# Optimization experiments

Hardware: AMD Instinct MI355X
Metric: run time of the kernel (lower is better)

Reference implementation:

```python
import jax, jax.numpy as jnp
import numpy as np

BLOCKSIZE = 128
KEEPER = 128


def setup_inputs() -> dict:
    key = jax.random.key(0)
    ks = jax.random.split(key, 8)
    S, H = 2048, 4096
    n_nonout = H - KEEPER          # 3968
    nb = n_nonout // BLOCKSIZE     # 31 low-precision blocks
    return {
        "x": jax.random.normal(ks[0], (1, S, H), dtype=jnp.float32),
        "weight": jax.random.normal(ks[1], (H, H), dtype=jnp.float32),   # [out, in]
        "scales": jax.random.uniform(ks[2], (H, n_nonout), dtype=jnp.float32),
        "keep_scales": jax.random.uniform(ks[3], (H, 1), dtype=jnp.float32),
        "inp_scales_lo": jax.random.uniform(ks[4], (S, nb), dtype=jnp.float32),
        "inp_scales_hi": jax.random.uniform(ks[5], (S, 1), dtype=jnp.float32),
        "inp_base_lo": jax.random.uniform(ks[6], (S, nb), dtype=jnp.float32),
        "inp_base_hi": jax.random.uniform(ks[7], (S, 1), dtype=jnp.float32),
    }


def reference(x, weight, scales, keep_scales, inp_scales_lo, inp_scales_hi,
              inp_base_lo, inp_base_hi):
    # Faithful vectorization of QLinearLayer._forward (channel_group == 0, bias None).
    bs, S, H = x.shape
    xs = x[0]                      # [S, H]  (bs == 1 assert in original)
    W = weight.T                   # [H, O]
    n_nonout = H - KEEPER
    nb = n_nonout // BLOCKSIZE
    O = W.shape[1]

    # Per-block weight scales: scales[:, i1] for each block start i1 -> [nb, O]
    w_blk_scales = scales[:, 0:n_nonout:BLOCKSIZE].T              # [nb, O]

    # Blockwise outer-product scaling fused into the operands:
    # y[s,o] = sum_n sc_lo[s,n] * ws[n,o] * (x_block_n @ W_block_n)[s,o]
    x_lo = xs[:, :n_nonout].reshape(S, nb, BLOCKSIZE) * inp_scales_lo[:, :, None]
    W_lo = W[:n_nonout, :].reshape(nb, BLOCKSIZE, O) * w_blk_scales[:, None, :]
    y = x_lo.reshape(S, n_nonout) @ W_lo.reshape(n_nonout, O)     # [S, O]

    # int8 keeper channels (high-precision path)
    hi_scales = inp_scales_hi @ keep_scales.T                      # [S, O]
    y_hi = xs[:, n_nonout:] @ W[n_nonout:, :]                      # [S, O]
    y = y + y_hi * hi_scales

    return y.reshape(bs, S, O)
```

## Files before the change

### kernel.cpp

```cpp
#include <hip/hip_runtime.h>

#define S_DIM 2048
#define K_DIM 4096
#define O_DIM 4096
#define NNON  3968
#define NB    31

#define XBLK 8192
#define WBLK 16384

typedef __bf16 bf16x8 __attribute__((ext_vector_type(8)));
typedef float  f32x4  __attribute__((ext_vector_type(4)));

__device__ __forceinline__ unsigned short f2bf(float f) {
    union { float f; unsigned u; } v; v.f = f;
    unsigned r = v.u + 0x7FFFu + ((v.u >> 16) & 1u);
    return (unsigned short)(r >> 16);
}

__global__ __launch_bounds__(256) void prepass(const float* __restrict__ x,
                                               const float* __restrict__ sc_lo,
                                               const float* __restrict__ sc_hi,
                                               const float* __restrict__ w,
                                               const float* __restrict__ scales,
                                               const float* __restrict__ keep,
                                               unsigned short* __restrict__ A,
                                               unsigned short* __restrict__ B)
{
    const int b = blockIdx.x;
    if (b < XBLK) {
        int idx = b * 256 + threadIdx.x;
        int s = idx >> 10;
        int k = (idx & 1023) << 2;
        float4 v = ((const float4*)x)[idx];
        float sc = (k < NNON) ? sc_lo[s * NB + (k >> 7)] : sc_hi[s];
        ushort4 o;
        o.x = f2bf(v.x * sc); o.y = f2bf(v.y * sc);
        o.z = f2bf(v.z * sc); o.w = f2bf(v.w * sc);
        ((ushort4*)A)[idx] = o;
    } else {
        int idx = (b - XBLK) * 256 + threadIdx.x;
        int o = idx >> 10;
        int k = (idx & 1023) << 2;
        float4 v = ((const float4*)w)[idx];
        float sc = (k < NNON) ? scales[(size_t)o * NNON + ((k >> 7) << 7)] : keep[o];
        ushort4 r;
        r.x = f2bf(v.x * sc); r.y = f2bf(v.y * sc);
        r.z = f2bf(v.z * sc); r.w = f2bf(v.w * sc);
        ((ushort4*)B)[idx] = r;
    }
}

#define BM 128
#define BN 256
#define BK 64
#define NT (K_DIM / BK)

#define GPTR(p) ((__attribute__((address_space(1))) unsigned int*)(p))
#define LPTR(p) ((__attribute__((address_space(3))) unsigned int*)(p))

__device__ __forceinline__ void vm_wait6() { asm volatile("s_waitcnt vmcnt(6)" ::: "memory"); }
__device__ __forceinline__ void vm_wait0() { asm volatile("s_waitcnt vmcnt(0)" ::: "memory"); }
__device__ __forceinline__ void wg_barrier() {
    asm volatile("" ::: "memory");
    __builtin_amdgcn_s_barrier();
    asm volatile("" ::: "memory");
}

__global__ __launch_bounds__(512, 2) void gemm_bt(const unsigned short* __restrict__ A,
                                                  const unsigned short* __restrict__ B,
                                                  float* __restrict__ C)
{
    __shared__ __align__(16) unsigned short As[2][BM * BK];
    __shared__ __align__(16) unsigned short Bs[2][BN * BK];

    const int tid  = threadIdx.x;
    const int wave = tid >> 6;
    const int lane = tid & 63;
    const int quad = lane >> 4;
    const int l16  = lane & 15;

    const int wg = blockIdx.x;
    const int sw = (wg & 7) * 32 + (wg >> 3);
    const int bm = (sw >> 4) * BM;
    const int bn = (sw & 15) * BN;

    const int wm = (wave >> 2) * 64;
    const int wn = (wave & 3) * 64;

    const int r8 = lane >> 3;
    const int q8 = lane & 7;
    const unsigned short* Ag = A + (size_t)(bm + wave * 8 + r8) * K_DIM + ((q8 ^ r8) << 3);
    const unsigned short* Bg = B + (size_t)(bn + wave * 8 + r8) * K_DIM + ((q8 ^ r8) << 3);

    f32x4 acc[4][4];
    #pragma unroll
    for (int i = 0; i < 4; ++i)
        #pragma unroll
        for (int j = 0; j < 4; ++j)
            acc[i][j] = (f32x4){0.f, 0.f, 0.f, 0.f};

    auto stageA = [&](int t) {
        unsigned short* dst = &As[t & 1][wave * 8 * BK];
        #pragma unroll
        for (int s = 0; s < 2; ++s)
            __builtin_amdgcn_global_load_lds(GPTR(Ag + (size_t)(s * 64) * K_DIM + t * BK),
                                             LPTR(dst + s * 64 * BK), 16, 0, 0);
    };
    auto stageB = [&](int t) {
        unsigned short* dst = &Bs[t & 1][wave * 8 * BK];
        #pragma unroll
        for (int s = 0; s < 4; ++s)
            __builtin_amdgcn_global_load_lds(GPTR(Bg + (size_t)(s * 64) * K_DIM + t * BK),
                                             LPTR(dst + s * 64 * BK), 16, 0, 0);
    };

    stageA(0); stageB(0);
    stageA(1); stageB(1);
    vm_wait6();
    wg_barrier();

    #pragma unroll 2
    for (int t = 0; t < NT; ++t) {
        const int cur = t & 1;
        const unsigned short* asb = As[cur];
        const unsigned short* bsb = Bs[cur];

        bf16x8 af[2][4], b01[2][2];
        #pragma unroll
        for (int ks = 0; ks < 2; ++ks) {
            #pragma unroll
            for (int i = 0; i < 4; ++i)
                af[ks][i] = *(const bf16x8*)&asb[(wm + i * 16 + l16) * BK +
                                                 (((ks * 4 + quad) ^ (l16 & 7)) << 3)];
            #pragma unroll
            for (int j = 0; j < 2; ++j)
                b01[ks][j] = *(const bf16x8*)&bsb[(wn + j * 16 + l16) * BK +
                                                  (((ks * 4 + quad) ^ (l16 & 7)) << 3)];
        }
        wg_barrier();
        if (t < NT - 2) stageA(t + 2);

        __builtin_amdgcn_s_setprio(1);
        #pragma unroll
        for (int ks = 0; ks < 2; ++ks)
            #pragma unroll
            for (int i = 0; i < 4; ++i)
                #pragma unroll
                for (int j = 0; j < 2; ++j)
                    acc[i][j] = __builtin_amdgcn_mfma_f32_16x16x32_bf16(af[ks][i], b01[ks][j],
                                                                        acc[i][j], 0, 0, 0);
        __builtin_amdgcn_s_setprio(0);

        bf16x8 b23[2][2];
        #pragma unroll
        for (int ks = 0; ks < 2; ++ks)
            #pragma unroll
            for (int j = 0; j < 2; ++j)
                b23[ks][j] = *(const bf16x8*)&bsb[(wn + (j + 2) * 16 + l16) * BK +
                                                  (((ks * 4 + quad) ^ (l16 & 7)) << 3)];
        wg_barrier();
        if (t < NT - 2) stageB(t + 2);

        __builtin_amdgcn_s_setprio(1);
        #pragma unroll
        for (int ks = 0; ks < 2; ++ks)
            #pragma unroll
            for (int i = 0; i < 4; ++i)
                #pragma unroll
                for (int j = 0; j < 2; ++j)
                    acc[i][j + 2] = __builtin_amdgcn_mfma_f32_16x16x32_bf16(af[ks][i], b23[ks][j],
                                                                            acc[i][j + 2], 0, 0, 0);
        __builtin_amdgcn_s_setprio(0);

        if (t < NT - 2)       vm_wait6();
        else if (t == NT - 2) vm_wait0();
        wg_barrier();
    }

    #pragma unroll
    for (int i = 0; i < 4; ++i)
        #pragma unroll
        for (int j = 0; j < 4; ++j) {
            const int col = bn + wn + j * 16 + l16;
            #pragma unroll
            for (int r = 0; r < 4; ++r) {
                const int row = bm + wm + i * 16 + quad * 4 + r;
                C[(size_t)row * O_DIM + col] = acc[i][j][r];
            }
        }
}

extern "C" void kernel_launch(void* const* d_in, const int* in_sizes, int n_in,
                              void* d_out, int out_size, void* d_ws, size_t ws_size,
                              hipStream_t stream) {
    const float* x      = (const float*)d_in[0];
    const float* weight = (const float*)d_in[1];
    const float* scales = (const float*)d_in[2];
    const float* keep   = (const float*)d_in[3];
    const float* sc_lo  = (const float*)d_in[4];
    const float* sc_hi  = (const float*)d_in[5];

    unsigned short* A = (unsigned short*)d_ws;
    unsigned short* B = A + (size_t)S_DIM * K_DIM;

    prepass<<<XBLK + WBLK, 256, 0, stream>>>(x, sc_lo, sc_hi, weight, scales, keep, A, B);

    dim3 grid(256);
    gemm_bt<<<grid, 512, 0, stream>>>(A, B, (float*)d_out);
}
```

Baseline: 245.2 us.

## Use 256x256 GEMM tiles with split-K over two slices and atomic accumulation

Grows the GEMM tile from 128x256 to 256x256, so each wave computes an 8x4 MFMA accumulator block, and splits K into two 2048-wide slices to keep 256 workgroups. The partial results are combined with atomic float adds into an output zeroed by an added memset. The inner loop is restaged into four MFMA phases with interleaved LDS loads of half-tiles. The larger tile raises arithmetic intensity per LDS byte, at the cost of doubling accumulator registers (risking occupancy), the atomic output traffic, and an extra memset.

```diff
diff --git a/kernel.cpp b/kernel.cpp
--- a/kernel.cpp
+++ b/kernel.cpp
@@ -51,10 +51,11 @@
     }
 }
 
-#define BM 128
+#define BM 256
 #define BN 256
 #define BK 64
-#define NT (K_DIM / BK)
+#define KSLICE 2048
+#define NTK (KSLICE / BK)
 
 #define GPTR(p) ((__attribute__((address_space(1))) unsigned int*)(p))
 #define LPTR(p) ((__attribute__((address_space(3))) unsigned int*)(p))
@@ -80,113 +81,148 @@
     const int quad = lane >> 4;
     const int l16  = lane & 15;
 
-    const int wg = blockIdx.x;
-    const int sw = (wg & 7) * 32 + (wg >> 3);
-    const int bm = (sw >> 4) * BM;
-    const int bn = (sw & 15) * BN;
-
-    const int wm = (wave >> 2) * 64;
+    const int wg   = blockIdx.x;
+    const int sw   = (wg & 7) * 32 + (wg >> 3);
+    const int tile = sw >> 1;
+    const int ksl  = sw & 1;
+    const int bm = (tile >> 4) * BM;
+    const int bn = (tile & 15) * BN;
+    const int kbase = ksl * KSLICE;
+
+    const int wm = (wave >> 2) * 128;
     const int wn = (wave & 3) * 64;
 
     const int r8 = lane >> 3;
     const int q8 = lane & 7;
-    const unsigned short* Ag = A + (size_t)(bm + wave * 8 + r8) * K_DIM + ((q8 ^ r8) << 3);
-    const unsigned short* Bg = B + (size_t)(bn + wave * 8 + r8) * K_DIM + ((q8 ^ r8) << 3);
-
-    f32x4 acc[4][4];
+    const unsigned short* Ag = A + (size_t)(bm + wave * 8 + r8) * K_DIM + kbase + ((q8 ^ r8) << 3);
+    const unsigned short* Bg = B + (size_t)(bn + wave * 8 + r8) * K_DIM + kbase + ((q8 ^ r8) << 3);
+
+    f32x4 acc[8][4];
     #pragma unroll
-    for (int i = 0; i < 4; ++i)
+    for (int i = 0; i < 8; ++i)
         #pragma unroll
         for (int j = 0; j < 4; ++j)
             acc[i][j] = (f32x4){0.f, 0.f, 0.f, 0.f};
 
-    auto stageA = [&](int t) {
-        unsigned short* dst = &As[t & 1][wave * 8 * BK];
+    auto stageA = [&](int v, int h) {
+        unsigned short* dst = &As[v & 1][(h * 128 + wave * 8) * BK];
+        const unsigned short* src = Ag + (size_t)(h * 128) * K_DIM + v * BK;
         #pragma unroll
         for (int s = 0; s < 2; ++s)
-            __builtin_amdgcn_global_load_lds(GPTR(Ag + (size_t)(s * 64) * K_DIM + t * BK),
+            __builtin_amdgcn_global_load_lds(GPTR(src + (size_t)(s * 64) * K_DIM),
                                              LPTR(dst + s * 64 * BK), 16, 0, 0);
     };
-    auto stageB = [&](int t) {
-        unsigned short* dst = &Bs[t & 1][wave * 8 * BK];
-        #pragma unroll
-        for (int s = 0; s < 4; ++s)
-            __builtin_amdgcn_global_load_lds(GPTR(Bg + (size_t)(s * 64) * K_DIM + t * BK),
+    auto stageB = [&](int v, int h) {
+        unsigned short* dst = &Bs[v & 1][(h * 128 + wave * 8) * BK];
+        const unsigned short* src = Bg + (size_t)(h * 128) * K_DIM + v * BK;
+        #pragma unroll
+        for (int s = 0; s < 2; ++s)
+            __builtin_amdgcn_global_load_lds(GPTR(src + (size_t)(s * 64) * K_DIM),
                                              LPTR(dst + s * 64 * BK), 16, 0, 0);
     };
 
-    stageA(0); stageB(0);
-    stageA(1); stageB(1);
+    stageA(0, 0); stageA(0, 1); stageB(0, 0); stageB(0, 1);
+    stageB(1, 0); stageB(1, 1); stageA(1, 0);
     vm_wait6();
     wg_barrier();
 
+    const int co0 = ((quad)     ^ (l16 & 7)) << 3;
+    const int co1 = ((4 + quad) ^ (l16 & 7)) << 3;
+
     #pragma unroll 2
-    for (int t = 0; t < NT; ++t) {
-        const int cur = t & 1;
-        const unsigned short* asb = As[cur];
-        const unsigned short* bsb = Bs[cur];
-
-        bf16x8 af[2][4], b01[2][2];
-        #pragma unroll
-        for (int ks = 0; ks < 2; ++ks) {
-            #pragma unroll
-            for (int i = 0; i < 4; ++i)
-                af[ks][i] = *(const bf16x8*)&asb[(wm + i * 16 + l16) * BK +
-                                                 (((ks * 4 + quad) ^ (l16 & 7)) << 3)];
-            #pragma unroll
-            for (int j = 0; j < 2; ++j)
-                b01[ks][j] = *(const bf16x8*)&bsb[(wn + j * 16 + l16) * BK +
-                                                  (((ks * 4 + quad) ^ (l16 & 7)) << 3)];
-        }
-        wg_barrier();
-        if (t < NT - 2) stageA(t + 2);
-
-        __builtin_amdgcn_s_setprio(1);
-        #pragma unroll
-        for (int ks = 0; ks < 2; ++ks)
-            #pragma unroll
-            for (int i = 0; i < 4; ++i)
-                #pragma unroll
-                for (int j = 0; j < 2; ++j)
-                    acc[i][j] = __builtin_amdgcn_mfma_f32_16x16x32_bf16(af[ks][i], b01[ks][j],
+    for (int u = 0; u < NTK; ++u) {
+        const unsigned short* asb = As[u & 1];
+        const unsigned short* bsb = Bs[u & 1];
+        bf16x8 Aa[2][4], Ab[2][4], B0f[2][2], B1f[2][2];
+
+        #pragma unroll
+        for (int i = 0; i < 4; ++i) {
+            Aa[0][i] = *(const bf16x8*)&asb[(wm + i * 16 + l16) * BK + co0];
+            Aa[1][i] = *(const bf16x8*)&asb[(wm + i * 16 + l16) * BK + co1];
+        }
+        #pragma unroll
+        for (int j = 0; j < 2; ++j) {
+            B0f[0][j] = *(const bf16x8*)&bsb[(wn + j * 16 + l16) * BK + co0];
+            B0f[1][j] = *(const bf16x8*)&bsb[(wn + j * 16 + l16) * BK + co1];
+        }
+        if (u + 1 < NTK) stageA(u + 1, 1);
+        wg_barrier();
+        __builtin_amdgcn_s_setprio(1);
+        #pragma unroll
+        for (int ks = 0; ks < 2; ++ks)
+            #pragma unroll
+            for (int i = 0; i < 4; ++i)
+                #pragma unroll
+                for (int j = 0; j < 2; ++j)
+                    acc[i][j] = __builtin_amdgcn_mfma_f32_16x16x32_bf16(Aa[ks][i], B0f[ks][j],
                                                                         acc[i][j], 0, 0, 0);
         __builtin_amdgcn_s_setprio(0);
-
-        bf16x8 b23[2][2];
-        #pragma unroll
-        for (int ks = 0; ks < 2; ++ks)
-            #pragma unroll
-            for (int j = 0; j < 2; ++j)
-                b23[ks][j] = *(const bf16x8*)&bsb[(wn + (j + 2) * 16 + l16) * BK +
-                                                  (((ks * 4 + quad) ^ (l16 & 7)) << 3)];
-        wg_barrier();
-        if (t < NT - 2) stageB(t + 2);
-
-        __builtin_amdgcn_s_setprio(1);
-        #pragma unroll
-        for (int ks = 0; ks < 2; ++ks)
-            #pragma unroll
-            for (int i = 0; i < 4; ++i)
-                #pragma unroll
-                for (int j = 0; j < 2; ++j)
-                    acc[i][j + 2] = __builtin_amdgcn_mfma_f32_16x16x32_bf16(af[ks][i], b23[ks][j],
+        wg_barrier();
+
+        #pragma unroll
+        for (int j = 0; j < 2; ++j) {
+            B1f[0][j] = *(const bf16x8*)&bsb[(wn + (j + 2) * 16 + l16) * BK + co0];
+            B1f[1][j] = *(const bf16x8*)&bsb[(wn + (j + 2) * 16 + l16) * BK + co1];
+        }
+        if (u + 2 < NTK) stageB(u + 2, 0);
+        wg_barrier();
+        __builtin_amdgcn_s_setprio(1);
+        #pragma unroll
+        for (int ks = 0; ks < 2; ++ks)
+            #pragma unroll
+            for (int i = 0; i < 4; ++i)
+                #pragma unroll
+                for (int j = 0; j < 2; ++j)
+                    acc[i][j + 2] = __builtin_amdgcn_mfma_f32_16x16x32_bf16(Aa[ks][i], B1f[ks][j],
                                                                             acc[i][j + 2], 0, 0, 0);
         __builtin_amdgcn_s_setprio(0);
-
-        if (t < NT - 2)       vm_wait6();
-        else if (t == NT - 2) vm_wait0();
+        wg_barrier();
+
+        #pragma unroll
+        for (int i = 0; i < 4; ++i) {
+            Ab[0][i] = *(const bf16x8*)&asb[(wm + (i + 4) * 16 + l16) * BK + co0];
+            Ab[1][i] = *(const bf16x8*)&asb[(wm + (i + 4) * 16 + l16) * BK + co1];
+        }
+        if (u + 2 < NTK) stageB(u + 2, 1);
+        wg_barrier();
+        __builtin_amdgcn_s_setprio(1);
+        #pragma unroll
+        for (int ks = 0; ks < 2; ++ks)
+            #pragma unroll
+            for (int i = 0; i < 4; ++i)
+                #pragma unroll
+                for (int j = 0; j < 2; ++j)
+                    acc[i + 4][j + 2] = __builtin_amdgcn_mfma_f32_16x16x32_bf16(Ab[ks][i], B1f[ks][j],
+                                                                                acc[i + 4][j + 2], 0, 0, 0);
+        __builtin_amdgcn_s_setprio(0);
+        wg_barrier();
+
+        if (u + 2 < NTK) stageA(u + 2, 0);
+        wg_barrier();
+        __builtin_amdgcn_s_setprio(1);
+        #pragma unroll
+        for (int ks = 0; ks < 2; ++ks)
+            #pragma unroll
+            for (int i = 0; i < 4; ++i)
+                #pragma unroll
+                for (int j = 0; j < 2; ++j)
+                    acc[i + 4][j] = __builtin_amdgcn_mfma_f32_16x16x32_bf16(Ab[ks][i], B0f[ks][j],
+                                                                            acc[i + 4][j], 0, 0, 0);
+        __builtin_amdgcn_s_setprio(0);
+        if (u < NTK - 2)       vm_wait6();
+        else if (u == NTK - 2) vm_wait0();
         wg_barrier();
     }
 
     #pragma unroll
-    for (int i = 0; i < 4; ++i)
+    for (int i = 0; i < 8; ++i)
         #pragma unroll
         for (int j = 0; j < 4; ++j) {
             const int col = bn + wn + j * 16 + l16;
             #pragma unroll
             for (int r = 0; r < 4; ++r) {
                 const int row = bm + wm + i * 16 + quad * 4 + r;
-                C[(size_t)row * O_DIM + col] = acc[i][j][r];
+                unsafeAtomicAdd(&C[(size_t)row * O_DIM + col], acc[i][j][r]);
             }
         }
 }
@@ -204,6 +240,7 @@
     unsigned short* A = (unsigned short*)d_ws;
     unsigned short* B = A + (size_t)S_DIM * K_DIM;
 
+    hipMemsetAsync(d_out, 0, (size_t)S_DIM * O_DIM * sizeof(float), stream);
     prepass<<<XBLK + WBLK, 256, 0, stream>>>(x, sc_lo, sc_hi, weight, scales, keep, A, B);
 
     dim3 grid(256);
```

Result: slower. 283.1 us (+15.5%).

## Restructure GEMM wave tiling to 1x8 and rework LDS pipeline schedule

Applied to the files above, without the earlier changes.

Changes the per-wave tile from 64x64 in a 2x4 wave grid to 128x32 in a 1x8 grid, so every wave reads the whole A tile and its own 32-column slice of B. The main loop is rewritten to handle two K tiles per iteration, with explicit buffer indices, split A and B staging points, and lgkmcnt waits before each MFMA phase. The goal is to interleave global-to-LDS loads with compute more finely. In exchange, per-wave LDS read traffic for A rises and the barriers become denser.

```diff
diff --git a/kernel.cpp b/kernel.cpp
--- a/kernel.cpp
+++ b/kernel.cpp
@@ -54,13 +54,15 @@
 #define BM 128
 #define BN 256
 #define BK 64
-#define NT (K_DIM / BK)
+#define NTILES (K_DIM / BK)
+#define NIT (NTILES / 2)
 
 #define GPTR(p) ((__attribute__((address_space(1))) unsigned int*)(p))
 #define LPTR(p) ((__attribute__((address_space(3))) unsigned int*)(p))
 
-__device__ __forceinline__ void vm_wait6() { asm volatile("s_waitcnt vmcnt(6)" ::: "memory"); }
+__device__ __forceinline__ void vm_wait4() { asm volatile("s_waitcnt vmcnt(4)" ::: "memory"); }
 __device__ __forceinline__ void vm_wait0() { asm volatile("s_waitcnt vmcnt(0)" ::: "memory"); }
+__device__ __forceinline__ void lgkm0()    { asm volatile("s_waitcnt lgkmcnt(0)" ::: "memory"); }
 __device__ __forceinline__ void wg_barrier() {
     asm volatile("" ::: "memory");
     __builtin_amdgcn_s_barrier();
@@ -85,108 +87,152 @@
     const int bm = (sw >> 4) * BM;
     const int bn = (sw & 15) * BN;
 
-    const int wm = (wave >> 2) * 64;
-    const int wn = (wave & 3) * 64;
+    const int wn = wave * 32;
 
     const int r8 = lane >> 3;
     const int q8 = lane & 7;
     const unsigned short* Ag = A + (size_t)(bm + wave * 8 + r8) * K_DIM + ((q8 ^ r8) << 3);
     const unsigned short* Bg = B + (size_t)(bn + wave * 8 + r8) * K_DIM + ((q8 ^ r8) << 3);
 
-    f32x4 acc[4][4];
+    f32x4 acc[8][2];
     #pragma unroll
-    for (int i = 0; i < 4; ++i)
-        #pragma unroll
-        for (int j = 0; j < 4; ++j)
-            acc[i][j] = (f32x4){0.f, 0.f, 0.f, 0.f};
-
-    auto stageA = [&](int t) {
-        unsigned short* dst = &As[t & 1][wave * 8 * BK];
+    for (int ii = 0; ii < 8; ++ii)
+        #pragma unroll
+        for (int j = 0; j < 2; ++j)
+            acc[ii][j] = (f32x4){0.f, 0.f, 0.f, 0.f};
+
+    auto stageA = [&](int buf, int t) {
+        unsigned short* dst = &As[buf][(wave * 8) * BK];
+        const unsigned short* src = Ag + t * BK;
         #pragma unroll
         for (int s = 0; s < 2; ++s)
-            __builtin_amdgcn_global_load_lds(GPTR(Ag + (size_t)(s * 64) * K_DIM + t * BK),
+            __builtin_amdgcn_global_load_lds(GPTR(src + (size_t)(s * 64) * K_DIM),
                                              LPTR(dst + s * 64 * BK), 16, 0, 0);
     };
-    auto stageB = [&](int t) {
-        unsigned short* dst = &Bs[t & 1][wave * 8 * BK];
-        #pragma unroll
-        for (int s = 0; s < 4; ++s)
-            __builtin_amdgcn_global_load_lds(GPTR(Bg + (size_t)(s * 64) * K_DIM + t * BK),
+    auto stageB = [&](int buf, int t, int h) {
+        unsigned short* dst = &Bs[buf][(h * 128 + wave * 8) * BK];
+        const unsigned short* src = Bg + (size_t)(h * 128) * K_DIM + t * BK;
+        #pragma unroll
+        for (int s = 0; s < 2; ++s)
+            __builtin_amdgcn_global_load_lds(GPTR(src + (size_t)(s * 64) * K_DIM),
                                              LPTR(dst + s * 64 * BK), 16, 0, 0);
     };
 
-    stageA(0); stageB(0);
-    stageA(1); stageB(1);
-    vm_wait6();
+    stageB(0, 0, 0); stageB(0, 0, 1); stageA(0, 0);
+    stageB(1, 1, 0); stageB(1, 1, 1);
+    vm_wait4();
     wg_barrier();
 
-    #pragma unroll 2
-    for (int t = 0; t < NT; ++t) {
-        const int cur = t & 1;
-        const unsigned short* asb = As[cur];
-        const unsigned short* bsb = Bs[cur];
-
-        bf16x8 af[2][4], b01[2][2];
-        #pragma unroll
-        for (int ks = 0; ks < 2; ++ks) {
-            #pragma unroll
-            for (int i = 0; i < 4; ++i)
-                af[ks][i] = *(const bf16x8*)&asb[(wm + i * 16 + l16) * BK +
-                                                 (((ks * 4 + quad) ^ (l16 & 7)) << 3)];
-            #pragma unroll
-            for (int j = 0; j < 2; ++j)
-                b01[ks][j] = *(const bf16x8*)&bsb[(wn + j * 16 + l16) * BK +
-                                                  (((ks * 4 + quad) ^ (l16 & 7)) << 3)];
-        }
-        wg_barrier();
-        if (t < NT - 2) stageA(t + 2);
-
-        __builtin_amdgcn_s_setprio(1);
-        #pragma unroll
-        for (int ks = 0; ks < 2; ++ks)
-            #pragma unroll
-            for (int i = 0; i < 4; ++i)
-                #pragma unroll
-                for (int j = 0; j < 2; ++j)
-                    acc[i][j] = __builtin_amdgcn_mfma_f32_16x16x32_bf16(af[ks][i], b01[ks][j],
-                                                                        acc[i][j], 0, 0, 0);
-        __builtin_amdgcn_s_setprio(0);
-
-        bf16x8 b23[2][2];
-        #pragma unroll
-        for (int ks = 0; ks < 2; ++ks)
-            #pragma unroll
-            for (int j = 0; j < 2; ++j)
-                b23[ks][j] = *(const bf16x8*)&bsb[(wn + (j + 2) * 16 + l16) * BK +
-                                                  (((ks * 4 + quad) ^ (l16 & 7)) << 3)];
-        wg_barrier();
-        if (t < NT - 2) stageB(t + 2);
-
-        __builtin_amdgcn_s_setprio(1);
-        #pragma unroll
-        for (int ks = 0; ks < 2; ++ks)
-            #pragma unroll
-            for (int i = 0; i < 4; ++i)
-                #pragma unroll
-                for (int j = 0; j < 2; ++j)
-                    acc[i][j + 2] = __builtin_amdgcn_mfma_f32_16x16x32_bf16(af[ks][i], b23[ks][j],
-                                                                            acc[i][j + 2], 0, 0, 0);
-        __builtin_amdgcn_s_setprio(0);
-
-        if (t < NT - 2)       vm_wait6();
-        else if (t == NT - 2) vm_wait0();
+    const int co0 = ((quad)     ^ (l16 & 7)) << 3;
+    const int co1 = ((4 + quad) ^ (l16 & 7)) << 3;
+
+    #pragma unroll 1
+    for (int it = 0; it < NIT; ++it) {
+        const bool more = (it < NIT - 1);
+        const int O  = 2 * it + 1;
+        const int E2 = 2 * it + 2;
+        const int O2 = 2 * it + 3;
+
+        bf16x8 alo[2][4], ahi[2][4], bf[2][2];
+
+        #pragma unroll
+        for (int ii = 0; ii < 4; ++ii) {
+            alo[0][ii] = *(const bf16x8*)&As[0][(ii * 16 + l16) * BK + co0];
+            alo[1][ii] = *(const bf16x8*)&As[0][(ii * 16 + l16) * BK + co1];
+        }
+        #pragma unroll
+        for (int j = 0; j < 2; ++j) {
+            bf[0][j] = *(const bf16x8*)&Bs[0][(wn + j * 16 + l16) * BK + co0];
+            bf[1][j] = *(const bf16x8*)&Bs[0][(wn + j * 16 + l16) * BK + co1];
+        }
+        stageA(1, O);
+        wg_barrier(); lgkm0();
+        __builtin_amdgcn_s_setprio(1);
+        #pragma unroll
+        for (int ks = 0; ks < 2; ++ks)
+            #pragma unroll
+            for (int ii = 0; ii < 4; ++ii)
+                #pragma unroll
+                for (int j = 0; j < 2; ++j)
+                    acc[ii][j] = __builtin_amdgcn_mfma_f32_16x16x32_bf16(alo[ks][ii], bf[ks][j],
+                                                                         acc[ii][j], 0, 0, 0);
+        __builtin_amdgcn_s_setprio(0);
+        wg_barrier();
+
+        #pragma unroll
+        for (int ii = 0; ii < 4; ++ii) {
+            ahi[0][ii] = *(const bf16x8*)&As[0][((ii + 4) * 16 + l16) * BK + co0];
+            ahi[1][ii] = *(const bf16x8*)&As[0][((ii + 4) * 16 + l16) * BK + co1];
+        }
+        if (more) { stageB(0, E2, 0); stageB(0, E2, 1); }
+        wg_barrier(); lgkm0();
+        __builtin_amdgcn_s_setprio(1);
+        #pragma unroll
+        for (int ks = 0; ks < 2; ++ks)
+            #pragma unroll
+            for (int ii = 0; ii < 4; ++ii)
+                #pragma unroll
+                for (int j = 0; j < 2; ++j)
+                    acc[ii + 4][j] = __builtin_amdgcn_mfma_f32_16x16x32_bf16(ahi[ks][ii], bf[ks][j],
+                                                                             acc[ii + 4][j], 0, 0, 0);
+        __builtin_amdgcn_s_setprio(0);
+        if (more) vm_wait4(); else vm_wait0();
+        wg_barrier();
+
+        #pragma unroll
+        for (int ii = 0; ii < 4; ++ii) {
+            alo[0][ii] = *(const bf16x8*)&As[1][(ii * 16 + l16) * BK + co0];
+            alo[1][ii] = *(const bf16x8*)&As[1][(ii * 16 + l16) * BK + co1];
+        }
+        #pragma unroll
+        for (int j = 0; j < 2; ++j) {
+            bf[0][j] = *(const bf16x8*)&Bs[1][(wn + j * 16 + l16) * BK + co0];
+            bf[1][j] = *(const bf16x8*)&Bs[1][(wn + j * 16 + l16) * BK + co1];
+        }
+        if (more) stageA(0, E2);
+        wg_barrier(); lgkm0();
+        __builtin_amdgcn_s_setprio(1);
+        #pragma unroll
+        for (int ks = 0; ks < 2; ++ks)
+            #pragma unroll
+            for (int ii = 0; ii < 4; ++ii)
+                #pragma unroll
+                for (int j = 0; j < 2; ++j)
+                    acc[ii][j] = __builtin_amdgcn_mfma_f32_16x16x32_bf16(alo[ks][ii], bf[ks][j],
+                                                                         acc[ii][j], 0, 0, 0);
+        __builtin_amdgcn_s_setprio(0);
+        wg_barrier();
+
+        #pragma unroll
+        for (int ii = 0; ii < 4; ++ii) {
+            ahi[0][ii] = *(const bf16x8*)&As[1][((ii + 4) * 16 + l16) * BK + co0];
+            ahi[1][ii] = *(const bf16x8*)&As[1][((ii + 4) * 16 + l16) * BK + co1];
+        }
+        if (more) { stageB(1, O2, 0); stageB(1, O2, 1); }
+        wg_barrier(); lgkm0();
+        __builtin_amdgcn_s_setprio(1);
+        #pragma unroll
+        for (int ks = 0; ks < 2; ++ks)
+            #pragma unroll
+            for (int ii = 0; ii < 4; ++ii)
+                #pragma unroll
+                for (int j = 0; j < 2; ++j)
+                    acc[ii + 4][j] = __builtin_amdgcn_mfma_f32_16x16x32_bf16(ahi[ks][ii], bf[ks][j],
+                                                                             acc[ii + 4][j], 0, 0, 0);
+        __builtin_amdgcn_s_setprio(0);
+        if (more) vm_wait4();
         wg_barrier();
     }
 
     #pragma unroll
-    for (int i = 0; i < 4; ++i)
-        #pragma unroll
-        for (int j = 0; j < 4; ++j) {
+    for (int ii = 0; ii < 8; ++ii)
+        #pragma unroll
+        for (int j = 0; j < 2; ++j) {
             const int col = bn + wn + j * 16 + l16;
             #pragma unroll
             for (int r = 0; r < 4; ++r) {
-                const int row = bm + wm + i * 16 + quad * 4 + r;
-                C[(size_t)row * O_DIM + col] = acc[i][j][r];
+                const int row = bm + ii * 16 + quad * 4 + r;
+                C[(size_t)row * O_DIM + col] = acc[ii][j][r];
             }
         }
 }
```

New measurement: 257.6 us. 5.1% more time.
